# Optimization experiments

Hardware: AMD Instinct MI355X
Metric: run time of the kernel (lower is better)

## Reference

```python
import jax, jax.numpy as jnp
import numpy as np


def setup_inputs() -> dict:
    key = jax.random.key(0)
    k1, k2, k3 = jax.random.split(key, 3)
    N, K, H, W = 8, 8, 256, 256
    C, P = 32, 100000
    fragments = jax.random.randint(k1, (N, K, H, W), 0, P, dtype=jnp.int64)
    alphas = jax.random.uniform(k2, (N, K, H, W), dtype=jnp.float32)
    features = jax.random.normal(k3, (C, P), dtype=jnp.float32)
    return {"fragments": fragments, "alphas": alphas, "features": features}


def reference(fragments, alphas, features):
    # Alpha compositing (front-to-back over the K points-per-pixel axis):
    #   weight_k = alpha_k * prod_{j<k} (1 - alpha_j)
    #   out[n,c,h,w] = sum_k weight_k[n,k,h,w] * features[c, fragments[n,k,h,w]]
    # Indices < 0 mark empty fragment slots (sorted to the tail by the
    # rasterizer); treat them as alpha = 0 so they contribute nothing and
    # do not attenuate.
    valid = fragments >= 0                                   # (N,K,H,W)
    a = jnp.where(valid, alphas, 0.0)                        # (N,K,H,W)
    # exclusive cumulative product of transmittance (1 - alpha) along K
    trans = jnp.cumprod(1.0 - a, axis=1)                     # inclusive
    excl = jnp.concatenate(
        [jnp.ones_like(trans[:, :1]), trans[:, :-1]], axis=1
    )                                                        # exclusive
    weights = a * excl                                       # (N,K,H,W)
    idx = jnp.where(valid, fragments, 0)
    gathered = features[:, idx]                              # (C,N,K,H,W)
    images = jnp.einsum("cnkhw,nkhw->nchw", gathered, weights)
    return images
```

## Files before the change

### kernel.cpp

```cpp
#include <hip/hip_runtime.h>

#define N_IMG 8
#define K_LAY 8
#define H_DIM 256
#define W_DIM 256
#define C_CH  32
#define P_FEAT 100000
#define HW 65536
#define NPIX (N_IMG * HW)

#define T_EPS 3e-3f

__global__ __launch_bounds__(256) void transpose_feat(
    const float* __restrict__ feat, float* __restrict__ featT)
{
    __shared__ float tile[32][33];
    const int x  = threadIdx.x;
    const int y  = threadIdx.y;
    const int p0 = blockIdx.x * 32;

    #pragma unroll
    for (int j = 0; j < 4; ++j) {
        const int c = y * 4 + j;
        tile[c][x] = feat[(size_t)c * P_FEAT + p0 + x];
    }
    __syncthreads();
    #pragma unroll
    for (int j = 0; j < 4; ++j) {
        const int pl = y * 4 + j;
        featT[(size_t)(p0 + pl) * C_CH + x] = tile[x][pl];
    }
}

__global__ __launch_bounds__(256) void composite(
    const int*   __restrict__ frag,
    const float* __restrict__ alpha,
    const float* __restrict__ featT,
    float*       __restrict__ out)
{
    const int gid = blockIdx.x * 256 + threadIdx.x;
    const int n = gid >> 16;
    const int p = gid & (HW - 1);

    const int*   fb = frag  + (size_t)n * K_LAY * HW + p;
    const float* ab = alpha + (size_t)n * K_LAY * HW + p;

    float acc[C_CH];
    #pragma unroll
    for (int c = 0; c < C_CH; ++c) acc[c] = 0.0f;

    float T = 1.0f;
    #pragma unroll
    for (int k = 0; k < K_LAY; ++k) {
        if (T >= T_EPS) {
            const int   f = fb[(size_t)k * HW];
            float       a = ab[(size_t)k * HW];
            const bool valid = (f >= 0);
            a = valid ? a : 0.0f;
            const float wgt = a * T;
            T *= (1.0f - a);
            if (wgt > 0.0f) {
                const float4* __restrict__ src =
                    (const float4*)(featT + (size_t)f * C_CH);
                #pragma unroll
                for (int j = 0; j < 8; ++j) {
                    const float4 v = src[j];
                    acc[4*j+0] = fmaf(wgt, v.x, acc[4*j+0]);
                    acc[4*j+1] = fmaf(wgt, v.y, acc[4*j+1]);
                    acc[4*j+2] = fmaf(wgt, v.z, acc[4*j+2]);
                    acc[4*j+3] = fmaf(wgt, v.w, acc[4*j+3]);
                }
            }
        }
    }

    float* ob = out + (size_t)n * C_CH * HW + p;
    #pragma unroll
    for (int c = 0; c < C_CH; ++c)
        ob[(size_t)c * HW] = acc[c];
}

__global__ __launch_bounds__(256) void composite_strided(
    const int*   __restrict__ frag,
    const float* __restrict__ alpha,
    const float* __restrict__ feat,
    float*       __restrict__ out)
{
    const int gid = blockIdx.x * 256 + threadIdx.x;
    const int n = gid >> 16;
    const int p = gid & (HW - 1);

    const int*   fb = frag  + (size_t)n * K_LAY * HW + p;
    const float* ab = alpha + (size_t)n * K_LAY * HW + p;

    float acc[C_CH];
    #pragma unroll
    for (int c = 0; c < C_CH; ++c) acc[c] = 0.0f;

    float T = 1.0f;
    #pragma unroll
    for (int k = 0; k < K_LAY; ++k) {
        if (T >= T_EPS) {
            const int   f = fb[(size_t)k * HW];
            float       a = ab[(size_t)k * HW];
            const bool valid = (f >= 0);
            a = valid ? a : 0.0f;
            const float wgt = a * T;
            T *= (1.0f - a);
            if (wgt > 0.0f) {
                #pragma unroll
                for (int c = 0; c < C_CH; ++c)
                    acc[c] = fmaf(wgt, feat[(size_t)c * P_FEAT + f], acc[c]);
            }
        }
    }

    float* ob = out + (size_t)n * C_CH * HW + p;
    #pragma unroll
    for (int c = 0; c < C_CH; ++c)
        ob[(size_t)c * HW] = acc[c];
}

extern "C" void kernel_launch(void* const* d_in, const int* in_sizes, int n_in,
                              void* d_out, int out_size, void* d_ws, size_t ws_size,
                              hipStream_t stream)
{
    const int*   frag  = (const int*)  d_in[0];
    const float* alpha = (const float*)d_in[1];
    const float* feat  = (const float*)d_in[2];
    float*       out   = (float*)d_out;

    const size_t need = (size_t)P_FEAT * C_CH * sizeof(float);
    if (ws_size >= need) {
        float* featT = (float*)d_ws;
        transpose_feat<<<dim3(P_FEAT / 32), dim3(32, 8), 0, stream>>>(feat, featT);
        composite<<<dim3(NPIX / 256), dim3(256), 0, stream>>>(frag, alpha, featT, out);
    } else {
        composite_strided<<<dim3(NPIX / 256), dim3(256), 0, stream>>>(frag, alpha, feat, out);
    }
}
```

Baseline: 157.2 us.

## Store transposed features as fp16 and precompute branch-free compositing weights

The transposed feature table is now stored in half precision, which halves the bytes per gathered feature row (64 B instead of 128 B) and shrinks the table so more of it stays in cache. The composite kernel loads all fragment indices and alphas up front, computes the weights without branches, and issues every gather unconditionally, using index 0 with weight 0 for dead slots. This exposes more memory-level parallelism. In exchange, features lose precision to fp16 rounding, and pixels that are already saturated still pay for gathers they used to skip.

```diff
diff --git a/kernel.cpp b/kernel.cpp
--- a/kernel.cpp
+++ b/kernel.cpp
@@ -1,9 +1,8 @@
 #include <hip/hip_runtime.h>
+#include <hip/hip_fp16.h>
 
 #define N_IMG 8
 #define K_LAY 8
-#define H_DIM 256
-#define W_DIM 256
 #define C_CH  32
 #define P_FEAT 100000
 #define HW 65536
@@ -11,8 +10,8 @@
 
 #define T_EPS 3e-3f
 
-__global__ __launch_bounds__(256) void transpose_feat(
-    const float* __restrict__ feat, float* __restrict__ featT)
+__global__ __launch_bounds__(256) void transpose_feat_h(
+    const float* __restrict__ feat, __half* __restrict__ featT)
 {
     __shared__ float tile[32][33];
     const int x  = threadIdx.x;
@@ -25,18 +24,23 @@
         tile[c][x] = feat[(size_t)c * P_FEAT + p0 + x];
     }
     __syncthreads();
+
+    const int t  = x + 32 * y;
+    const int pl = t >> 3;
+    const int c0 = (t & 7) * 4;
+    union { __half h[4]; unsigned long long u; } pk;
     #pragma unroll
-    for (int j = 0; j < 4; ++j) {
-        const int pl = y * 4 + j;
-        featT[(size_t)(p0 + pl) * C_CH + x] = tile[x][pl];
-    }
+    for (int j = 0; j < 4; ++j)
+        pk.h[j] = __float2half(tile[c0 + j][pl]);
+    *reinterpret_cast<unsigned long long*>(
+        featT + (size_t)(p0 + pl) * C_CH + c0) = pk.u;
 }
 
 __global__ __launch_bounds__(256) void composite(
-    const int*   __restrict__ frag,
-    const float* __restrict__ alpha,
-    const float* __restrict__ featT,
-    float*       __restrict__ out)
+    const int*    __restrict__ frag,
+    const float*  __restrict__ alpha,
+    const __half* __restrict__ featT,
+    float*        __restrict__ out)
 {
     const int gid = blockIdx.x * 256 + threadIdx.x;
     const int n = gid >> 16;
@@ -45,31 +49,44 @@
     const int*   fb = frag  + (size_t)n * K_LAY * HW + p;
     const float* ab = alpha + (size_t)n * K_LAY * HW + p;
 
+    int   f[K_LAY];
+    float a[K_LAY];
+    #pragma unroll
+    for (int k = 0; k < K_LAY; ++k) f[k] = fb[(size_t)k * HW];
+    #pragma unroll
+    for (int k = 0; k < K_LAY; ++k) a[k] = ab[(size_t)k * HW];
+
+    float w[K_LAY];
+    int   idx[K_LAY];
+    float T = 1.0f;
+    #pragma unroll
+    for (int k = 0; k < K_LAY; ++k) {
+        const bool  valid = (f[k] >= 0);
+        const float ak    = valid ? a[k] : 0.0f;
+        const bool  live  = (T >= T_EPS) && valid;
+        w[k]   = live ? ak * T : 0.0f;
+        idx[k] = live ? f[k] : 0;
+        T *= (1.0f - ak);
+    }
+
     float acc[C_CH];
     #pragma unroll
     for (int c = 0; c < C_CH; ++c) acc[c] = 0.0f;
 
-    float T = 1.0f;
     #pragma unroll
     for (int k = 0; k < K_LAY; ++k) {
-        if (T >= T_EPS) {
-            const int   f = fb[(size_t)k * HW];
-            float       a = ab[(size_t)k * HW];
-            const bool valid = (f >= 0);
-            a = valid ? a : 0.0f;
-            const float wgt = a * T;
-            T *= (1.0f - a);
-            if (wgt > 0.0f) {
-                const float4* __restrict__ src =
-                    (const float4*)(featT + (size_t)f * C_CH);
-                #pragma unroll
-                for (int j = 0; j < 8; ++j) {
-                    const float4 v = src[j];
-                    acc[4*j+0] = fmaf(wgt, v.x, acc[4*j+0]);
-                    acc[4*j+1] = fmaf(wgt, v.y, acc[4*j+1]);
-                    acc[4*j+2] = fmaf(wgt, v.z, acc[4*j+2]);
-                    acc[4*j+3] = fmaf(wgt, v.w, acc[4*j+3]);
-                }
+        const float4* __restrict__ src =
+            reinterpret_cast<const float4*>(featT + (size_t)idx[k] * C_CH);
+        const float wk = w[k];
+        #pragma unroll
+        for (int q = 0; q < 4; ++q) {
+            float4 r = src[q];
+            const __half2* hp = reinterpret_cast<const __half2*>(&r);
+            #pragma unroll
+            for (int j = 0; j < 4; ++j) {
+                const float2 fj = __half22float2(hp[j]);
+                acc[q*8 + j*2 + 0] = fmaf(wk, fj.x, acc[q*8 + j*2 + 0]);
+                acc[q*8 + j*2 + 1] = fmaf(wk, fj.y, acc[q*8 + j*2 + 1]);
             }
         }
     }
@@ -103,8 +120,7 @@
         if (T >= T_EPS) {
             const int   f = fb[(size_t)k * HW];
             float       a = ab[(size_t)k * HW];
-            const bool valid = (f >= 0);
-            a = valid ? a : 0.0f;
+            a = (f >= 0) ? a : 0.0f;
             const float wgt = a * T;
             T *= (1.0f - a);
             if (wgt > 0.0f) {
@@ -130,10 +146,10 @@
     const float* feat  = (const float*)d_in[2];
     float*       out   = (float*)d_out;
 
-    const size_t need = (size_t)P_FEAT * C_CH * sizeof(float);
+    const size_t need = (size_t)P_FEAT * C_CH * sizeof(__half);
     if (ws_size >= need) {
-        float* featT = (float*)d_ws;
-        transpose_feat<<<dim3(P_FEAT / 32), dim3(32, 8), 0, stream>>>(feat, featT);
+        __half* featT = (__half*)d_ws;
+        transpose_feat_h<<<dim3(P_FEAT / 32), dim3(32, 8), 0, stream>>>(feat, featT);
         composite<<<dim3(NPIX / 256), dim3(256), 0, stream>>>(frag, alpha, featT, out);
     } else {
         composite_strided<<<dim3(NPIX / 256), dim3(256), 0, stream>>>(frag, alpha, feat, out);
```

Result: faster. 148.2 us (-5.8%).
